# Kernel tuning notes

Hardware: AMD Instinct MI355X
Metric: run time of the kernel (lower is better)

The kernel has to match this reference:

```python
import jax, jax.numpy as jnp
import numpy as np

B, S, D = 16, 2048, 1024


def setup_inputs() -> dict:
    key = jax.random.key(0)
    ks = jax.random.split(key, 12)
    s = 1.0 / np.sqrt(D)
    s2 = 1.0 / np.sqrt(4 * D)
    return {
        "token_embeddings": jax.random.normal(ks[0], (B, S, D), dtype=jnp.float32),
        "attention_mask": jax.random.randint(ks[1], (B, S), 0, 2, dtype=jnp.int32),
        # linear weights stored as [in, out]
        "Wq": jax.random.uniform(ks[2], (D, D), jnp.float32, -s, s),
        "bq": jnp.zeros((D,), jnp.float32),
        "Wk": jax.random.uniform(ks[3], (D, D), jnp.float32, -s, s),
        "bk": jnp.zeros((D,), jnp.float32),
        "Wv": jax.random.uniform(ks[4], (D, D), jnp.float32, -s, s),
        "bv": jnp.zeros((D,), jnp.float32),
        "W1": jax.random.uniform(ks[5], (D, 4 * D), jnp.float32, -s, s),
        "b1": jnp.zeros((4 * D,), jnp.float32),
        "W2": jax.random.uniform(ks[6], (4 * D, D), jnp.float32, -s2, s2),
        "b2": jnp.zeros((D,), jnp.float32),
    }


def reference(token_embeddings, attention_mask, Wq, bq, Wk, bk, Wv, bv, W1, b1, W2, b2):
    d = token_embeddings.shape[-1]
    q = token_embeddings @ Wq + bq          # [B,S,D]
    k = token_embeddings @ Wk + bk          # [B,S,D]
    v = token_embeddings @ Wv + bv          # [B,S,D]
    scores = jnp.einsum("bqd,bkd->bqk", q, k) / jnp.sqrt(jnp.float32(d))  # [B,S,S]
    scores = jnp.where(attention_mask[:, None, :] == 0, -jnp.inf, scores)
    weights = jax.nn.softmax(scores, axis=-1)
    attn = jnp.einsum("bqk,bkd->bqd", weights, v)  # [B,S,D]
    pooled = attn.mean(axis=1)                      # [B,D]
    h = jax.nn.relu(pooled @ W1 + b1)               # [B,4D]
    return jnp.tanh(h @ W2 + b2)                    # [B,D]
```

## Files before the change

### kernel.cpp

```cpp
#include <hip/hip_runtime.h>
#include <hip/hip_bf16.h>

constexpr int B_ = 16;
constexpr int S_ = 2048;
constexpr int D_ = 1024;
constexpr int C_ = 1280;
constexpr long long BSD = (long long)B_ * S_ * D_;

typedef unsigned short u16;
typedef __bf16 bf16x8 __attribute__((ext_vector_type(8)));
typedef float    f32x4 __attribute__((ext_vector_type(4)));
typedef unsigned short usx8 __attribute__((ext_vector_type(8)));
typedef unsigned short usx4 __attribute__((ext_vector_type(4)));

__device__ inline u16 f2b(float f) {
  unsigned u = __float_as_uint(f);
  u = (u + 0x7fffu + ((u >> 16) & 1u)) >> 16;
  return (u16)u;
}
__device__ inline float b2f(u16 v) { return __uint_as_float(((unsigned)v) << 16); }

__device__ __forceinline__ void gll16(const void* g, void* l) {
  __builtin_amdgcn_global_load_lds(
      (const __attribute__((address_space(1))) void*)g,
      (__attribute__((address_space(3))) void*)l, 16, 0, 0);
}

__device__ __forceinline__ void vmwait0() {
  asm volatile("s_waitcnt vmcnt(0)" ::: "memory");
  __builtin_amdgcn_sched_barrier(0);
}
__device__ __forceinline__ void lgkm0w() {
  asm volatile("s_waitcnt lgkmcnt(0)" ::: "memory");
  __builtin_amdgcn_sched_barrier(0);
}
__device__ __forceinline__ void barrier_pin() {
  __builtin_amdgcn_sched_barrier(0);
  __builtin_amdgcn_s_barrier();
  __builtin_amdgcn_sched_barrier(0);
}

__global__ __launch_bounds__(256) void k_prep(
    const float* __restrict__ X, u16* __restrict__ Xb,
    const float* __restrict__ Wq, const float* __restrict__ Wk, const float* __restrict__ Wv,
    const float* __restrict__ bq, const float* __restrict__ bk, const float* __restrict__ bv,
    const int* __restrict__ mask, u16* __restrict__ Wt,
    float* __restrict__ biasQKV, int* __restrict__ map, int* __restrict__ counts) {
  __shared__ float tile[32][33];
  __shared__ int ts[256];
  const int bid = blockIdx.x;
  const int tid = threadIdx.x;
  if (bid < 16384) {
    size_t i = ((size_t)bid * 256 + tid) * 8;
    f32x4 a = *(const f32x4*)(X + i);
    f32x4 b = *(const f32x4*)(X + i + 4);
    usx8 o;
    o[0] = f2b(a[0]); o[1] = f2b(a[1]); o[2] = f2b(a[2]); o[3] = f2b(a[3]);
    o[4] = f2b(b[0]); o[5] = f2b(b[1]); o[6] = f2b(b[2]); o[7] = f2b(b[3]);
    *(usx8*)(Xb + i) = o;
  } else if (bid < 16384 + 3072) {
    const int wb = bid - 16384;
    const int z = wb >> 10, t = wb & 1023;
    const float* W = (z == 0) ? Wq : (z == 1 ? Wk : Wv);
    u16* dst = Wt + (size_t)z * D_ * D_;
    const int n0 = (t & 31) * 32, k0 = (t >> 5) * 32;
    const int tx = tid & 31, ty = tid >> 5;
    for (int r = ty; r < 32; r += 8)
      tile[r][tx] = W[(size_t)(k0 + r) * D_ + n0 + tx];
    __syncthreads();
    for (int r = ty; r < 32; r += 8)
      dst[(size_t)(n0 + r) * D_ + k0 + tx] = f2b(tile[tx][r]);
  } else if (bid == 16384 + 3072) {
    for (int x = tid; x < 3072; x += 256)
      biasQKV[x] = (x < 1024) ? bq[x] : (x < 2048 ? bk[x - 1024] : bv[x - 2048]);
  } else {
    const int b = bid - (16384 + 3073);
    const int* mrow = mask + b * S_;
    int lv[8]; int s = 0;
#pragma unroll
    for (int j = 0; j < 8; ++j) { lv[j] = (mrow[tid * 8 + j] != 0) ? 1 : 0; s += lv[j]; }
    ts[tid] = s;
    __syncthreads();
    for (int off = 1; off < 256; off <<= 1) {
      int v = (tid >= off) ? ts[tid - off] : 0;
      __syncthreads();
      ts[tid] += v;
      __syncthreads();
    }
    int pos = ts[tid] - s;
#pragma unroll
    for (int j = 0; j < 8; ++j) if (lv[j]) map[b * C_ + (pos++)] = tid * 8 + j;
    const int nb = ts[255];
    if (tid == 0) counts[b] = nb;
    for (int x = nb + tid; x < C_; x += 256) map[b * C_ + x] = 0;
  }
}

#define READ_A(DD, MQ)                                                    \
  _Pragma("unroll")                                                       \
  for (int f = 0; f < 4; ++f) {                                           \
    const int ad = (DD) + (MQ) * 8192 + A_pre + f * 1024;                 \
    a_[f][0] = *(const bf16x8*)(sm + ad);                                 \
    a_[f][1] = *(const bf16x8*)(sm + (ad ^ 32));                          \
  }

#define READ_B(DD, NQ)                                                    \
  _Pragma("unroll")                                                       \
  for (int n = 0; n < 2; ++n) {                                           \
    const int bd = (DD) + 16384 + (NQ) * 8192 + B_pre + n * 1024;         \
    b_[NQ][n][0] = *(const bf16x8*)(sm + bd);                             \
    b_[NQ][n][1] = *(const bf16x8*)(sm + (bd ^ 32));                      \
  }

#define MFMA_Q(IO, JO, BQ)                                                \
  __builtin_amdgcn_s_setprio(1);                                         \
  _Pragma("unroll")                                                       \
  for (int kk = 0; kk < 2; ++kk)                                          \
    _Pragma("unroll")                                                     \
    for (int f = 0; f < 4; ++f)                                           \
      _Pragma("unroll")                                                   \
      for (int n = 0; n < 2; ++n)                                         \
        acc[(IO) + f][(JO) + n] = __builtin_amdgcn_mfma_f32_16x16x32_bf16(\
            a_[f][kk], b_[BQ][n][kk], acc[(IO) + f][(JO) + n], 0, 0, 0);  \
  __builtin_amdgcn_s_setprio(0);

template <int MODE>
__global__ __launch_bounds__(512, 2) void k_gemm8(
    const u16* __restrict__ A, const u16* __restrict__ Bt,
    const float* __restrict__ bias, u16* __restrict__ C, u16* __restrict__ C2,
    const int* __restrict__ map, const int* __restrict__ counts, float scale) {
  extern __shared__ u16 sm[];
  constexpr int NT = 16;
  const int tid = threadIdx.x, lane = tid & 63, wave = tid >> 6;

  const int gx = gridDim.x, gy = gridDim.y;
  const int nwg = gx * gy * gridDim.z;
  const int orig = blockIdx.x + gx * (blockIdx.y + gy * blockIdx.z);
  const int cpx = nwg >> 3;
  const int tl = (orig & 7) * cpx + (orig >> 3);

  const u16* Az; const u16* Bz;
  int batch = 0, mtile = 0, bx, by;
  bool isQ = false;
  if constexpr (MODE == 0) {
    if (tl < 512) {
      isQ = true;
      bx = tl & 3; by = tl >> 2;
      Az = A; Bz = Bt;
    } else {
      const int i = tl - 512;
      bx = i & 7; by = i >> 3;
      batch = by / 5; mtile = by - batch * 5;
      if (mtile * 256 >= counts[batch]) return;
      Az = A + (size_t)batch * S_ * D_;
      Bz = Bt + (size_t)D_ * D_;
    }
  } else {
    bx = tl % gx;
    const int rest = tl / gx;
    by = rest % gy;
    batch = rest / gy;
    if (bx * 256 >= counts[batch]) return;
    Az = A + (size_t)batch * S_ * D_;
    Bz = Bt + (size_t)batch * C_ * D_;
  }
  const int wm_i = wave >> 2, wn_i = wave & 3;
  const int n0 = bx * 256;

  const int grow = tid >> 3;
  const int gslot = ((tid & 7) ^ ((tid >> 3) & 7)) * 8;
  const u16 *pAa0, *pAb0, *pAa1, *pAb1;
  if (MODE == 0 && !isQ) {
    const int* mp = map + batch * C_ + mtile * 256;
    pAa0 = Az + (size_t)mp[grow] * D_ + gslot;
    pAb0 = Az + (size_t)mp[grow + 64] * D_ + gslot;
    pAa1 = Az + (size_t)mp[grow + 128] * D_ + gslot;
    pAb1 = Az + (size_t)mp[grow + 192] * D_ + gslot;
  } else {
    const int m0 = by * 256;
    pAa0 = Az + (size_t)(m0 + grow) * D_ + gslot;
    pAb0 = pAa0 + (size_t)64 * D_;
    pAa1 = pAa0 + (size_t)128 * D_;
    pAb1 = pAa0 + (size_t)192 * D_;
  }
  const u16* pBa0 = Bz + (size_t)(n0 + grow) * D_ + gslot;
  const u16* pBb0 = pBa0 + (size_t)64 * D_;
  const u16* pBa1 = pBa0 + (size_t)128 * D_;
  const u16* pBb1 = pBa0 + (size_t)192 * D_;

  auto stage_part = [&](int t, int part) {
    const u16* ga = (part == 0) ? pAa0 : (part == 1) ? pAa1 : (part == 2) ? pBa0 : pBa1;
    const u16* gb = (part == 0) ? pAb0 : (part == 1) ? pAb1 : (part == 2) ? pBb0 : pBb1;
    u16* l0 = sm + (t & 1) * 32768 + part * 8192 + wave * 512;
    gll16(ga + t * 64, l0);
    gll16(gb + t * 64, l0 + 4096);
  };
  auto stage_all = [&](int t) {
    stage_part(t, 0); stage_part(t, 1); stage_part(t, 2); stage_part(t, 3);
  };

  const int r16 = lane & 15;
  const int s0k = (lane >> 4) ^ (lane & 7);
  const int A_pre = wm_i * 4096 + r16 * 64 + s0k * 8;
  const int B_pre = wn_i * 2048 + r16 * 64 + s0k * 8;

  f32x4 acc[8][4] = {};
  bf16x8 a_[4][2], b_[2][2][2];

  stage_all(0);
  vmwait0();
  barrier_pin();

#pragma unroll 1
  for (int t = 0; t < NT - 1; ++t) {
    const int DD = (t & 1) * 32768;
    READ_A(DD, 0) READ_B(DD, 0)
    __builtin_amdgcn_sched_barrier(0);
    stage_all(t + 1);
    barrier_pin(); lgkm0w();
    MFMA_Q(0, 0, 0)
    barrier_pin();
    READ_B(DD, 1)
    barrier_pin(); lgkm0w();
    MFMA_Q(0, 2, 1)
    barrier_pin();
    READ_A(DD, 1)
    barrier_pin(); lgkm0w();
    MFMA_Q(4, 2, 1)
    barrier_pin();
    vmwait0(); barrier_pin();
    MFMA_Q(4, 0, 0)
    barrier_pin();
  }
  {
    const int DD = ((NT - 1) & 1) * 32768;
    READ_A(DD, 0) READ_B(DD, 0)
    barrier_pin(); lgkm0w();
    MFMA_Q(0, 0, 0)
    barrier_pin();
    READ_B(DD, 1)
    barrier_pin(); lgkm0w();
    MFMA_Q(0, 2, 1)
    barrier_pin();
    READ_A(DD, 1)
    barrier_pin(); lgkm0w();
    MFMA_Q(4, 2, 1)
    barrier_pin();
    MFMA_Q(4, 0, 0)
  }

#pragma unroll
  for (int i = 0; i < 8; ++i) {
    const int MQ = i >> 2, f = i & 3;
    const int lrow = MQ * 128 + wm_i * 64 + f * 16 + ((lane >> 4) << 2);
#pragma unroll
    for (int j = 0; j < 4; ++j) {
      const int NQ = j >> 1, n = j & 1;
      const int col = n0 + NQ * 128 + wn_i * 32 + n * 16 + (lane & 15);
      if constexpr (MODE == 0) {
        if (isQ) {
          const float badd = bias[col];
          u16* cp = C + (size_t)(by * 256 + lrow) * 1024 + col;
#pragma unroll
          for (int r = 0; r < 4; ++r) cp[(size_t)r * 1024] = f2b(acc[i][j][r] + badd);
        } else {
          const float badd = bias[1024 + col];
          u16* cp = C2 + (size_t)(col >> 10) * ((size_t)16 * C_ * 1024)
                      + ((size_t)batch * C_ + mtile * 256 + lrow) * 1024 + (col & 1023);
#pragma unroll
          for (int r = 0; r < 4; ++r) cp[(size_t)r * 1024] = f2b(acc[i][j][r] + badd);
        }
      } else {
        u16* cp = C + ((size_t)batch * 2048 + by * 256 + lrow) * C_ + col;
#pragma unroll
        for (int r = 0; r < 4; ++r) cp[(size_t)r * C_] = f2b(acc[i][j][r] * scale);
      }
    }
  }
}

__global__ __launch_bounds__(256) void k_softmax_colsum(
    const u16* __restrict__ Sc, const int* __restrict__ counts,
    float* __restrict__ cpart) {
  __shared__ float colsum[C_];
  const int b = blockIdx.y, bi = blockIdx.x;
  const int tid = threadIdx.x, lane = tid & 63, wave = tid >> 6;
  for (int k = tid; k < C_; k += 256) colsum[k] = 0.0f;
  __syncthreads();

  const int nb = counts[b];
  const u16* base = Sc + ((size_t)b * 2048 + bi * 64 + wave * 16) * C_;
  const int c16 = lane * 16;
  const int c4 = 1024 + lane * 4;
  float csum[20];
#pragma unroll
  for (int i = 0; i < 20; i++) csum[i] = 0.0f;

  for (int rr = 0; rr < 16; rr++) {
    const u16* srow = base + (size_t)rr * C_;
    usx8 x0 = *(const usx8*)(srow + c16);
    usx8 x1 = *(const usx8*)(srow + c16 + 8);
    usx4 x2 = *(const usx4*)(srow + c4);
    float s[20];
    float m = -1e30f;
#pragma unroll
    for (int e = 0; e < 8; e++) {
      s[e] = (c16 + e < nb) ? b2f(x0[e]) : -1e30f;
      s[8 + e] = (c16 + 8 + e < nb) ? b2f(x1[e]) : -1e30f;
      m = fmaxf(m, fmaxf(s[e], s[8 + e]));
    }
#pragma unroll
    for (int e = 0; e < 4; e++) {
      s[16 + e] = (c4 + e < nb) ? b2f(x2[e]) : -1e30f;
      m = fmaxf(m, s[16 + e]);
    }
#pragma unroll
    for (int o = 1; o < 64; o <<= 1) m = fmaxf(m, __shfl_xor(m, o));
    float sum = 0.f;
#pragma unroll
    for (int i = 0; i < 20; i++) { s[i] = __expf(s[i] - m); sum += s[i]; }
#pragma unroll
    for (int o = 1; o < 64; o <<= 1) sum += __shfl_xor(sum, o);
    const float inv = 1.0f / (sum * (float)S_);
#pragma unroll
    for (int i = 0; i < 20; i++) csum[i] += s[i] * inv;
  }
#pragma unroll
  for (int i = 0; i < 16; i++) {
    const int e = (i + lane) & 15;
    atomicAdd(&colsum[c16 + e], csum[e]);
  }
#pragma unroll
  for (int i = 0; i < 4; i++) {
    const int e = (i + lane) & 3;
    atomicAdd(&colsum[c4 + e], csum[16 + e]);
  }
  __syncthreads();
  float* dst = cpart + ((size_t)b * 32 + bi) * C_;
  for (int k = tid; k < C_; k += 256) dst[k] = colsum[k];
}

__global__ __launch_bounds__(256) void k_cv(const float* __restrict__ cpart,
                                            const u16* __restrict__ Vc,
                                            float* __restrict__ pooled) {
  __shared__ float cl[128];
  const int b = blockIdx.y;
  const int k0 = blockIdx.x * 128;
  const int tid = threadIdx.x;
  if (tid < 128) {
    float s = 0.f;
    const float* p = cpart + (size_t)b * 32 * C_ + k0 + tid;
#pragma unroll 4
    for (int q = 0; q < 32; q++) s += p[(size_t)q * C_];
    cl[tid] = s;
  }
  __syncthreads();
  f32x4 acc = {};
  const u16* vb = Vc + ((size_t)b * C_ + k0) * 1024 + tid * 4;
  for (int k = 0; k < 128; k++) {
    const float w = cl[k];
    usx4 v = *(const usx4*)(vb + (size_t)k * 1024);
    acc[0] += w * b2f(v[0]);
    acc[1] += w * b2f(v[1]);
    acc[2] += w * b2f(v[2]);
    acc[3] += w * b2f(v[3]);
  }
#pragma unroll
  for (int q = 0; q < 4; q++) atomicAdd(&pooled[b * D_ + tid * 4 + q], acc[q]);
}

__global__ __launch_bounds__(256) void k_mlp1(const float* __restrict__ pooled,
                                              const float* __restrict__ W1,
                                              float* __restrict__ hpre) {
  __shared__ float ps[16][256];
  const int tid = threadIdx.x;
  const int j = blockIdx.x * 256 + tid;
  const int i0 = blockIdx.y * 256;
  for (int x = tid; x < 16 * 256; x += 256) {
    const int bb = x >> 8, ii = x & 255;
    ps[bb][ii] = pooled[bb * D_ + i0 + ii];
  }
  __syncthreads();
  float acc[16] = {};
  for (int i = 0; i < 256; i++) {
    const float w = W1[(size_t)(i0 + i) * (4 * D_) + j];
#pragma unroll
    for (int bb = 0; bb < 16; bb++) acc[bb] += ps[bb][i] * w;
  }
#pragma unroll
  for (int bb = 0; bb < 16; bb++) atomicAdd(&hpre[bb * (4 * D_) + j], acc[bb]);
}

__global__ __launch_bounds__(256) void k_mlp2(const float* __restrict__ hpre,
                                              const float* __restrict__ b1,
                                              const float* __restrict__ W2,
                                              float* __restrict__ outpre) {
  __shared__ float hs[16][256];
  const int tid = threadIdx.x;
  const int n = blockIdx.x * 256 + tid;
  const int i0 = blockIdx.y * 256;
  for (int x = tid; x < 16 * 256; x += 256) {
    const int bb = x >> 8, ii = x & 255;
    hs[bb][ii] = fmaxf(hpre[bb * (4 * D_) + i0 + ii] + b1[i0 + ii], 0.0f);
  }
  __syncthreads();
  float acc[16] = {};
  for (int i = 0; i < 256; i++) {
    const float w = W2[(size_t)(i0 + i) * D_ + n];
#pragma unroll
    for (int bb = 0; bb < 16; bb++) acc[bb] += hs[bb][i] * w;
  }
#pragma unroll
  for (int bb = 0; bb < 16; bb++) atomicAdd(&outpre[bb * D_ + n], acc[bb]);
}

__global__ void k_finish(const float* __restrict__ outpre, const float* __restrict__ b2,
                         float* __restrict__ out) {
  const int x = blockIdx.x * 256 + threadIdx.x;
  out[x] = tanhf(outpre[x] + b2[x & (D_ - 1)]);
}

extern "C" void kernel_launch(void* const* d_in, const int* in_sizes, int n_in,
                              void* d_out, int out_size, void* d_ws, size_t ws_size,
                              hipStream_t stream) {
  const float* X  = (const float*)d_in[0];
  const int* mask = (const int*)d_in[1];
  const float* Wq = (const float*)d_in[2];
  const float* bq = (const float*)d_in[3];
  const float* Wk = (const float*)d_in[4];
  const float* bk = (const float*)d_in[5];
  const float* Wv = (const float*)d_in[6];
  const float* bv = (const float*)d_in[7];
  const float* W1 = (const float*)d_in[8];
  const float* b1 = (const float*)d_in[9];
  const float* W2 = (const float*)d_in[10];
  const float* b2 = (const float*)d_in[11];
  float* out = (float*)d_out;

  char* ws = (char*)d_ws;
  size_t off = 0;
  auto alloc = [&](size_t bytes) -> void* {
    void* p = ws + off;
    off += (bytes + 255) & ~(size_t)255;
    return p;
  };
  u16* Qb  = (u16*)alloc(BSD * sizeof(u16));
  u16* KVc = (u16*)alloc((size_t)2 * 16 * C_ * D_ * sizeof(u16));
  u16* Kc  = KVc;
  u16* Vc  = KVc + (size_t)16 * C_ * D_;
  u16* ScX = (u16*)alloc((size_t)16 * 2048 * C_ * sizeof(u16));
  u16* Xb  = ScX;
  u16* Sc  = ScX;
  u16* Wt  = (u16*)alloc((size_t)3 * D_ * D_ * sizeof(u16));
  float* biasQKV = (float*)alloc(3 * D_ * sizeof(float));
  int* map    = (int*)alloc((size_t)16 * C_ * sizeof(int));
  int* counts = (int*)alloc(16 * sizeof(int));
  float* cpart  = (float*)alloc((size_t)32 * 16 * C_ * sizeof(float));
  float* pooled = (float*)alloc((size_t)B_ * D_ * sizeof(float));
  float* hpre   = (float*)alloc((size_t)B_ * 4 * D_ * sizeof(float));
  float* outpre = (float*)alloc((size_t)B_ * D_ * sizeof(float));
  (void)ws_size; (void)in_sizes; (void)n_in; (void)out_size;

  const size_t zero_bytes = (size_t)B_ * D_ * 4 + (size_t)B_ * 4 * D_ * 4 +
                            (size_t)B_ * D_ * 4;
  hipMemsetAsync(pooled, 0, zero_bytes, stream);

  k_prep<<<16384 + 3089, 256, 0, stream>>>(X, Xb, Wq, Wk, Wv, bq, bk, bv,
                                           mask, Wt, biasQKV, map, counts);

  k_gemm8<0><<<dim3(1152, 1, 1), 512, 131072, stream>>>(
      Xb, Wt, biasQKV, Qb, KVc, map, counts, 1.0f);

  k_gemm8<2><<<dim3(C_ / 256, 8, 16), 512, 131072, stream>>>(
      Qb, Kc, nullptr, Sc, nullptr, nullptr, counts, 0.03125f);

  k_softmax_colsum<<<dim3(32, B_), 256, 0, stream>>>(Sc, counts, cpart);
  k_cv<<<dim3(C_ / 128, B_), 256, 0, stream>>>(cpart, Vc, pooled);
  k_mlp1<<<dim3(16, 4), 256, 0, stream>>>(pooled, W1, hpre);
  k_mlp2<<<dim3(4, 16), 256, 0, stream>>>(hpre, b1, W2, outpre);
  k_finish<<<64, 256, 0, stream>>>(outpre, b2, out);
}
```

Baseline: 468.7 us.

## Interleave GEMM prefetch stages with MFMA phases and split MLP reductions finer

The GEMM main loop used to issue all four global-to-LDS prefetch parts for the next tile at once and then wait for every load before the last MFMA quarter. It now issues one part before each MFMA quarter and waits with partial vmcnt counts, so loads stay spread across the compute and the full drain is avoided. Separately, the two MLP kernels split the reduction dimension into chunks of 64 instead of 256, launching four times as many blocks to fill the GPU, at the cost of four times more atomicAdds. The partial-wait counts must match the order loads are issued in, or the loop risks reading LDS data that has not arrived yet.

```diff
diff --git a/kernel.cpp b/kernel.cpp
--- a/kernel.cpp
+++ b/kernel.cpp
@@ -26,6 +26,14 @@
       (__attribute__((address_space(3))) void*)l, 16, 0, 0);
 }
 
+__device__ __forceinline__ void vmwait4() {
+  asm volatile("s_waitcnt vmcnt(4)" ::: "memory");
+  __builtin_amdgcn_sched_barrier(0);
+}
+__device__ __forceinline__ void vmwait2() {
+  asm volatile("s_waitcnt vmcnt(2)" ::: "memory");
+  __builtin_amdgcn_sched_barrier(0);
+}
 __device__ __forceinline__ void vmwait0() {
   asm volatile("s_waitcnt vmcnt(0)" ::: "memory");
   __builtin_amdgcn_sched_barrier(0);
@@ -195,9 +203,6 @@
     gll16(ga + t * 64, l0);
     gll16(gb + t * 64, l0 + 4096);
   };
-  auto stage_all = [&](int t) {
-    stage_part(t, 0); stage_part(t, 1); stage_part(t, 2); stage_part(t, 3);
-  };
 
   const int r16 = lane & 15;
   const int s0k = (lane >> 4) ^ (lane & 7);
@@ -207,8 +212,8 @@
   f32x4 acc[8][4] = {};
   bf16x8 a_[4][2], b_[2][2][2];
 
-  stage_all(0);
-  vmwait0();
+  stage_part(0, 0); stage_part(0, 2); stage_part(0, 3); stage_part(0, 1);
+  vmwait4();
   barrier_pin();
 
 #pragma unroll 1
@@ -216,30 +221,35 @@
     const int DD = (t & 1) * 32768;
     READ_A(DD, 0) READ_B(DD, 0)
     __builtin_amdgcn_sched_barrier(0);
-    stage_all(t + 1);
-    barrier_pin(); lgkm0w();
+    stage_part(t + 1, 0);
+    vmwait4(); barrier_pin(); lgkm0w();
     MFMA_Q(0, 0, 0)
     barrier_pin();
     READ_B(DD, 1)
-    barrier_pin(); lgkm0w();
+    __builtin_amdgcn_sched_barrier(0);
+    stage_part(t + 1, 2);
+    vmwait4(); barrier_pin(); lgkm0w();
     MFMA_Q(0, 2, 1)
     barrier_pin();
     READ_A(DD, 1)
+    __builtin_amdgcn_sched_barrier(0);
+    stage_part(t + 1, 3);
     barrier_pin(); lgkm0w();
     MFMA_Q(4, 2, 1)
     barrier_pin();
-    vmwait0(); barrier_pin();
+    stage_part(t + 1, 1);
+    vmwait4(); barrier_pin();
     MFMA_Q(4, 0, 0)
     barrier_pin();
   }
   {
     const int DD = ((NT - 1) & 1) * 32768;
     READ_A(DD, 0) READ_B(DD, 0)
-    barrier_pin(); lgkm0w();
+    vmwait2(); barrier_pin(); lgkm0w();
     MFMA_Q(0, 0, 0)
     barrier_pin();
     READ_B(DD, 1)
-    barrier_pin(); lgkm0w();
+    vmwait0(); barrier_pin(); lgkm0w();
     MFMA_Q(0, 2, 1)
     barrier_pin();
     READ_A(DD, 1)
@@ -372,17 +382,17 @@
 __global__ __launch_bounds__(256) void k_mlp1(const float* __restrict__ pooled,
                                               const float* __restrict__ W1,
                                               float* __restrict__ hpre) {
-  __shared__ float ps[16][256];
+  __shared__ float ps[16][64];
   const int tid = threadIdx.x;
   const int j = blockIdx.x * 256 + tid;
-  const int i0 = blockIdx.y * 256;
-  for (int x = tid; x < 16 * 256; x += 256) {
-    const int bb = x >> 8, ii = x & 255;
+  const int i0 = blockIdx.y * 64;
+  for (int x = tid; x < 16 * 64; x += 256) {
+    const int bb = x >> 6, ii = x & 63;
     ps[bb][ii] = pooled[bb * D_ + i0 + ii];
   }
   __syncthreads();
   float acc[16] = {};
-  for (int i = 0; i < 256; i++) {
+  for (int i = 0; i < 64; i++) {
     const float w = W1[(size_t)(i0 + i) * (4 * D_) + j];
 #pragma unroll
     for (int bb = 0; bb < 16; bb++) acc[bb] += ps[bb][i] * w;
@@ -395,17 +405,17 @@
                                               const float* __restrict__ b1,
                                               const float* __restrict__ W2,
                                               float* __restrict__ outpre) {
-  __shared__ float hs[16][256];
+  __shared__ float hs[16][64];
   const int tid = threadIdx.x;
   const int n = blockIdx.x * 256 + tid;
-  const int i0 = blockIdx.y * 256;
-  for (int x = tid; x < 16 * 256; x += 256) {
-    const int bb = x >> 8, ii = x & 255;
+  const int i0 = blockIdx.y * 64;
+  for (int x = tid; x < 16 * 64; x += 256) {
+    const int bb = x >> 6, ii = x & 63;
     hs[bb][ii] = fmaxf(hpre[bb * (4 * D_) + i0 + ii] + b1[i0 + ii], 0.0f);
   }
   __syncthreads();
   float acc[16] = {};
-  for (int i = 0; i < 256; i++) {
+  for (int i = 0; i < 64; i++) {
     const float w = W2[(size_t)(i0 + i) * D_ + n];
 #pragma unroll
     for (int bb = 0; bb < 16; bb++) acc[bb] += hs[bb][i] * w;
@@ -476,7 +486,7 @@
 
   k_softmax_colsum<<<dim3(32, B_), 256, 0, stream>>>(Sc, counts, cpart);
   k_cv<<<dim3(C_ / 128, B_), 256, 0, stream>>>(cpart, Vc, pooled);
-  k_mlp1<<<dim3(16, 4), 256, 0, stream>>>(pooled, W1, hpre);
-  k_mlp2<<<dim3(4, 16), 256, 0, stream>>>(hpre, b1, W2, outpre);
+  k_mlp1<<<dim3(16, 16), 256, 0, stream>>>(pooled, W1, hpre);
+  k_mlp2<<<dim3(4, 64), 256, 0, stream>>>(hpre, b1, W2, outpre);
   k_finish<<<64, 256, 0, stream>>>(outpre, b2, out);
 }
```

Result: faster. 400.1 us (-14.6%).
